# Optimization experiments

Measured on AMD Instinct MI355X. Metric: run time of the kernel, lower is better.

## Reference

```python
import jax, jax.numpy as jnp
import numpy as np

B = 32; NPG = 500; N = B * NPG; E = 256000; F = 1024; OD = 128
DD = 80; TD = 32; NH = 4; DH = TD // NH; DFF = 128; NL = 2
LSUB = 128; MAXLEN = 4 * LSUB
NEG = -1e9; SLOPE = 0.01; EPS = 1e-5


def setup_inputs() -> dict:
    key = jax.random.key(0)
    ks = iter(jax.random.split(key, 64))
    nrm = lambda *s: jax.random.normal(next(ks), s, jnp.float32)
    w = lambda *s: nrm(*s) * 0.02
    inp = {}
    inp["pro1_x"] = nrm(N, F)
    inp["pro2_x"] = nrm(N, F)
    inp["pro1_edge_index"] = jax.random.randint(next(ks), (2, E), 0, N)
    inp["pro2_edge_index"] = jax.random.randint(next(ks), (2, E), 0, N)
    inp["pro1_batch"] = jnp.repeat(jnp.arange(B), NPG)
    inp["pro2_batch"] = jnp.repeat(jnp.arange(B), NPG)
    for nm in ("mas1_straight", "mas1_flipped", "mas2_straight", "mas2_flipped"):
        inp[nm] = nrm(B, LSUB, DD)
        inp[nm + "_lengths"] = jax.random.randint(next(ks), (B,), 1, LSUB + 1)
    inp["gcn1_w"] = w(F, F); inp["gcn1_b"] = jnp.zeros(F)
    inp["gcn2_w"] = w(F, F); inp["gcn2_b"] = jnp.zeros(F)
    inp["fc1_w"] = w(OD, F); inp["fc1_b"] = jnp.zeros(OD)
    inp["fc2_w"] = w(OD, F); inp["fc2_b"] = jnp.zeros(OD)
    inp["red_w"] = w(TD - 2, DD); inp["red_b"] = jnp.zeros(TD - 2)
    inp["attn_in_w"] = w(NL, 3 * TD, TD); inp["attn_in_b"] = jnp.zeros((NL, 3 * TD))
    inp["attn_out_w"] = w(NL, TD, TD); inp["attn_out_b"] = jnp.zeros((NL, TD))
    inp["ln1_w"] = jnp.ones((NL, TD)); inp["ln1_b"] = jnp.zeros((NL, TD))
    inp["ln2_w"] = jnp.ones((NL, TD)); inp["ln2_b"] = jnp.zeros((NL, TD))
    inp["ff1_w"] = w(NL, DFF, TD); inp["ff1_b"] = jnp.zeros((NL, DFF))
    inp["ff2_w"] = w(NL, TD, DFF); inp["ff2_b"] = jnp.zeros((NL, TD))
    inp["final_w"] = w(1, 2 * OD + TD); inp["final_b"] = jnp.zeros(1)
    return inp


def _leaky(v):
    return jnp.where(v >= 0, v, SLOPE * v)


def _gcn(x, ei, W, b):
    # GCNConv: x' = D^-1/2 (A + I) D^-1/2 (x @ W^T) + b
    sl = jnp.arange(N, dtype=ei.dtype)
    src = jnp.concatenate([ei[0], sl])
    dst = jnp.concatenate([ei[1], sl])
    deg = jax.ops.segment_sum(jnp.ones(src.shape[0], x.dtype), dst, N)
    dinv = jax.lax.rsqrt(deg)
    norm = (dinv[src] * dinv[dst])[:, None]
    h = x @ W.T
    return jax.ops.segment_sum(h[src] * norm, dst, N) + b


def _gmp(x, batch):
    # global mean pool per graph
    s = jax.ops.segment_sum(x, batch, B)
    c = jax.ops.segment_sum(jnp.ones(x.shape[0], x.dtype), batch, B)
    return s / c[:, None]


def _ln(x, w, b):
    m = x.mean(-1, keepdims=True)
    v = ((x - m) ** 2).mean(-1, keepdims=True)
    return (x - m) * jax.lax.rsqrt(v + EPS) * w + b


def _forward(pro1_x, pro1_edge_index, pro1_batch, pro2_x, pro2_edge_index, pro2_batch,
             mas1_straight, mas1_flipped, mas2_straight, mas2_flipped,
             mas1_straight_lengths, mas1_flipped_lengths, mas2_straight_lengths, mas2_flipped_lengths,
             gcn1_w, gcn1_b, fc1_w, fc1_b, gcn2_w, gcn2_b, fc2_w, fc2_b,
             red_w, red_b, attn_in_w, attn_in_b, attn_out_w, attn_out_b,
             ln1_w, ln1_b, ln2_w, ln2_b, ff1_w, ff1_b, ff2_w, ff2_b,
             final_w, final_b):
    # --- graph branches (dropout = identity at inference) ---
    x1 = _leaky(_gcn(pro1_x, pro1_edge_index, gcn1_w, gcn1_b))
    x1 = _leaky(_gmp(x1, pro1_batch) @ fc1_w.T + fc1_b)           # [B, OD]
    x2 = _leaky(_gcn(pro2_x, pro2_edge_index, gcn2_w, gcn2_b))
    x2 = _leaky(_gmp(x2, pro2_batch) @ fc2_w.T + fc2_b)           # [B, OD]

    # --- vectorized ragged pack: project, append indicators, scatter to offsets ---
    inds = ((1.0, 1.0), (0.0, 1.0), (1.0, 0.0), (0.0, 0.0))      # (straight, first)
    mas = (mas1_straight, mas1_flipped, mas2_straight, mas2_flipped)
    lens = (mas1_straight_lengths, mas1_flipped_lengths, mas2_straight_lengths, mas2_flipped_lengths)
    pos = jnp.arange(LSUB)
    brow = jnp.arange(B)[:, None]
    seq = jnp.zeros((B, MAXLEN, TD), jnp.float32)
    off = jnp.zeros((B,), lens[0].dtype)
    for m, l, (si, fi) in zip(mas, lens, inds):
        proj = m @ red_w.T + red_b                                # [B, LSUB, TD-2]
        ones = jnp.ones((B, LSUB, 1), jnp.float32)
        p = jnp.concatenate([proj, si * ones, fi * ones], -1)    # [B, LSUB, TD]
        valid = pos[None, :] < l[:, None]                        # [B, LSUB]
        idx = jnp.where(valid, off[:, None] + pos[None, :], 0)
        seq = seq.at[brow, idx].add(p * valid[..., None])
        off = off + l
    mask = jnp.arange(MAXLEN)[None, :] < off[:, None]            # [B, MAXLEN] True = valid

    # --- post-norm TransformerEncoder (relu FFN, key padding mask) ---
    x_t = seq
    for li in range(NL):
        qkv = x_t @ attn_in_w[li].T + attn_in_b[li]
        q, k, v = jnp.split(qkv, 3, axis=-1)
        q = q.reshape(B, MAXLEN, NH, DH)
        k = k.reshape(B, MAXLEN, NH, DH)
        v = v.reshape(B, MAXLEN, NH, DH)
        scores = jnp.einsum('bqhd,bkhd->bhqk', q, k) / np.float32(np.sqrt(DH))
        scores = jnp.where(mask[:, None, None, :], scores, NEG)
        attn = jax.nn.softmax(scores, axis=-1)
        o = jnp.einsum('bhqk,bkhd->bqhd', attn, v).reshape(B, MAXLEN, TD)
        o = o @ attn_out_w[li].T + attn_out_b[li]
        x_t = _ln(x_t + o, ln1_w[li], ln1_b[li])
        h = jax.nn.relu(x_t @ ff1_w[li].T + ff1_b[li]) @ ff2_w[li].T + ff2_b[li]
        x_t = _ln(x_t + h, ln2_w[li], ln2_b[li])

    mf = mask[..., None].astype(jnp.float32)
    mas_out = (x_t * mf).sum(1) / mf.sum(1)                      # masked mean [B, TD]

    combined = jnp.concatenate([x1, x2, mas_out], axis=1)        # [B, 2*OD + TD]
    return combined @ final_w.T + final_b                        # [B, 1]


def reference(pro1_x, pro1_edge_index, pro1_batch, pro2_x, pro2_edge_index, pro2_batch,
              mas1_straight, mas1_flipped, mas2_straight, mas2_flipped,
              mas1_straight_lengths, mas1_flipped_lengths, mas2_straight_lengths, mas2_flipped_lengths,
              gcn1_w, gcn1_b, fc1_w, fc1_b, gcn2_w, gcn2_b, fc2_w, fc2_b,
              red_w, red_b, attn_in_w, attn_in_b, attn_out_w, attn_out_b,
              ln1_w, ln1_b, ln2_w, ln2_b, ff1_w, ff1_b, ff2_w, ff2_b,
              final_w, final_b):
    return _forward(pro1_x, pro1_edge_index, pro1_batch, pro2_x, pro2_edge_index, pro2_batch,
                    mas1_straight, mas1_flipped, mas2_straight, mas2_flipped,
                    mas1_straight_lengths, mas1_flipped_lengths, mas2_straight_lengths, mas2_flipped_lengths,
                    gcn1_w, gcn1_b, fc1_w, fc1_b, gcn2_w, gcn2_b, fc2_w, fc2_b,
                    red_w, red_b, attn_in_w, attn_in_b, attn_out_w, attn_out_b,
                    ln1_w, ln1_b, ln2_w, ln2_b, ff1_w, ff1_b, ff2_w, ff2_b,
                    final_w, final_b)
```

## Files before the change

kernel.cpp:

```cpp
#include <hip/hip_runtime.h>
#include <stdint.h>

#define N_NODES 16000
#define MPAD_   16128
#define B_      32
#define NPG_    500
#define E_      256000
#define F_      1024
#define OD_     128
#define DD_     80
#define TD_     32
#define NH_     4
#define DH_     8
#define DFF_    128
#define LSUB_   128
#define MAXLEN_ 512
#define EPS_    1e-5f
#define SLOPE_  0.01f

typedef __bf16 bf16x8 __attribute__((ext_vector_type(8)));
typedef float  f32x4  __attribute__((ext_vector_type(4)));

__device__ __forceinline__ float leaky(float v) { return v >= 0.f ? v : SLOPE_ * v; }

__device__ __forceinline__ unsigned short f2bf(float f) {
  unsigned u = __float_as_uint(f);
  u += 0x7FFFu + ((u >> 16) & 1u);
  return (unsigned short)(u >> 16);
}
__device__ __forceinline__ float bf2f(unsigned short u) {
  return __uint_as_float((unsigned)u << 16);
}
__device__ __forceinline__ float bflo(unsigned u) { return __uint_as_float(u << 16); }
__device__ __forceinline__ float bfhi(unsigned u) { return __uint_as_float(u & 0xffff0000u); }
__device__ __forceinline__ unsigned pk2bf(float lo, float hi) {
  return (unsigned)f2bf(lo) | ((unsigned)f2bf(hi) << 16);
}

__device__ __forceinline__ void gld_lds16(const void* g, void* l) {
  __builtin_amdgcn_global_load_lds(
      (const __attribute__((address_space(1))) unsigned int*)g,
      (__attribute__((address_space(3))) unsigned int*)l, 16, 0, 0);
}

__global__ void k_f2bf2(const float* __restrict__ in0, const float* __restrict__ in1,
                        unsigned short* __restrict__ out0, unsigned short* __restrict__ out1,
                        int n4) {
  const float* in = blockIdx.y ? in1 : in0;
  unsigned short* out = blockIdx.y ? out1 : out0;
  int i = blockIdx.x * blockDim.x + threadIdx.x;
  int stride = gridDim.x * blockDim.x;
  for (; i < n4; i += stride) {
    float4 v = ((const float4*)in)[i];
    ushort4 o;
    o.x = f2bf(v.x); o.y = f2bf(v.y); o.z = f2bf(v.z); o.w = f2bf(v.w);
    ((ushort4*)out)[i] = o;
  }
}

#define LDSA(bf, ks, row) (*(const bf16x8*)&lds[(bf)*16384 + (ks)*8192 + (row)*32 + rs])
#define LDSB(bf, ks, row) (*(const bf16x8*)&lds[32768 + (bf)*16384 + (ks)*8192 + (row)*32 + rs])
#define STG_A(bf, R, kti) do { \
  gld_lds16(&Ag[(size_t)(mBase + (R) + r4) * 1024 + (kti) * 64 + c4],      &lds[(bf)*16384 + (R)*32 + t*8]); \
  gld_lds16(&Ag[(size_t)(mBase + (R) + r4) * 1024 + (kti) * 64 + 32 + c4], &lds[(bf)*16384 + 8192 + (R)*32 + t*8]); \
} while (0)
#define STG_B(bf, R, kti) do { \
  gld_lds16(&Bg[(size_t)(nBase + (R) + r4) * 1024 + (kti) * 64 + c4],      &lds[32768 + (bf)*16384 + (R)*32 + t*8]); \
  gld_lds16(&Bg[(size_t)(nBase + (R) + r4) * 1024 + (kti) * 64 + 32 + c4], &lds[32768 + (bf)*16384 + 8192 + (R)*32 + t*8]); \
} while (0)
#define RD_Q0(bf) do { \
  _Pragma("unroll") for (int mi = 0; mi < 4; ++mi) \
  _Pragma("unroll") for (int ks = 0; ks < 2; ++ks) \
    aLo[mi][ks] = LDSA(bf, ks, wrow * 128 + mi * 16 + l15); \
  _Pragma("unroll") for (int ni = 0; ni < 2; ++ni) \
  _Pragma("unroll") for (int ks = 0; ks < 2; ++ks) \
    bLo[ni][ks] = LDSB(bf, ks, wcol * 64 + ni * 16 + l15); \
} while (0)
#define RD_BHI(bf) do { \
  _Pragma("unroll") for (int ni = 0; ni < 2; ++ni) \
  _Pragma("unroll") for (int ks = 0; ks < 2; ++ks) \
    bHi[ni][ks] = LDSB(bf, ks, wcol * 64 + (2 + ni) * 16 + l15); \
} while (0)
#define RD_AHI(bf) do { \
  _Pragma("unroll") for (int mi = 0; mi < 4; ++mi) \
  _Pragma("unroll") for (int ks = 0; ks < 2; ++ks) \
    aHi[mi][ks] = LDSA(bf, ks, wrow * 128 + (4 + mi) * 16 + l15); \
} while (0)
#define MM_Q0() do { __builtin_amdgcn_s_setprio(1); \
  _Pragma("unroll") for (int mi = 0; mi < 4; ++mi) \
  _Pragma("unroll") for (int ni = 0; ni < 2; ++ni) \
  _Pragma("unroll") for (int ks = 0; ks < 2; ++ks) \
    acc[mi][ni] = __builtin_amdgcn_mfma_f32_16x16x32_bf16(aLo[mi][ks], bLo[ni][ks], acc[mi][ni], 0, 0, 0); \
  __builtin_amdgcn_s_setprio(0); } while (0)
#define MM_Q1() do { __builtin_amdgcn_s_setprio(1); \
  _Pragma("unroll") for (int mi = 0; mi < 4; ++mi) \
  _Pragma("unroll") for (int ni = 0; ni < 2; ++ni) \
  _Pragma("unroll") for (int ks = 0; ks < 2; ++ks) \
    acc[mi][2 + ni] = __builtin_amdgcn_mfma_f32_16x16x32_bf16(aLo[mi][ks], bHi[ni][ks], acc[mi][2 + ni], 0, 0, 0); \
  __builtin_amdgcn_s_setprio(0); } while (0)
#define MM_Q3() do { __builtin_amdgcn_s_setprio(1); \
  _Pragma("unroll") for (int mi = 0; mi < 4; ++mi) \
  _Pragma("unroll") for (int ni = 0; ni < 2; ++ni) \
  _Pragma("unroll") for (int ks = 0; ks < 2; ++ks) \
    acc[4 + mi][2 + ni] = __builtin_amdgcn_mfma_f32_16x16x32_bf16(aHi[mi][ks], bHi[ni][ks], acc[4 + mi][2 + ni], 0, 0, 0); \
  __builtin_amdgcn_s_setprio(0); } while (0)
#define MM_Q2() do { __builtin_amdgcn_s_setprio(1); \
  _Pragma("unroll") for (int mi = 0; mi < 4; ++mi) \
  _Pragma("unroll") for (int ni = 0; ni < 2; ++ni) \
  _Pragma("unroll") for (int ks = 0; ks < 2; ++ks) \
    acc[4 + mi][ni] = __builtin_amdgcn_mfma_f32_16x16x32_bf16(aHi[mi][ks], bLo[ni][ks], acc[4 + mi][ni], 0, 0, 0); \
  __builtin_amdgcn_s_setprio(0); } while (0)
#define BAR() do { __builtin_amdgcn_sched_barrier(0); __builtin_amdgcn_s_barrier(); \
                   __builtin_amdgcn_sched_barrier(0); } while (0)
#define LGKM0() do { asm volatile("s_waitcnt lgkmcnt(0)" ::: "memory"); \
                     __builtin_amdgcn_sched_barrier(0); } while (0)
#define VM4() do { asm volatile("s_waitcnt vmcnt(4)" ::: "memory"); } while (0)
#define VM0() do { asm volatile("s_waitcnt vmcnt(0)" ::: "memory"); } while (0)

__global__ __launch_bounds__(512, 2) void k_gemm256(const unsigned short* __restrict__ Ag,
                                                    const unsigned short* __restrict__ Bg,
                                                    unsigned short* __restrict__ Cg) {
  __shared__ short lds[65536];
  const int j  = blockIdx.x;
  const int x8 = j & 7;
  const int chunk = (x8 < 4) ? x8 * 32 : 128 + (x8 - 4) * 31;
  const int pos = chunk + (j >> 3);
  const int mb = pos >> 2, nb = pos & 3;
  const size_t g = blockIdx.z;
  Ag += g * (size_t)MPAD_ * 1024;
  Bg += g * (size_t)1024 * 1024;
  Cg += g * (size_t)MPAD_ * 1024;
  const int t = threadIdx.x;
  const int lane = t & 63, wave = t >> 6;
  const int wrow = wave >> 2, wcol = wave & 3;
  const int quad = lane >> 4, l15 = lane & 15;
  const int mBase = mb * 256, nBase = nb * 256;
  const int r4 = t >> 2;
  const int c4 = (((t & 3) - ((t >> 3) & 3)) & 3) * 8;
  const int rs = ((quad + (l15 >> 1)) & 3) * 8;

  f32x4 acc[8][4];
  f32x4 zero = {0.f, 0.f, 0.f, 0.f};
#pragma unroll
  for (int i = 0; i < 8; ++i)
#pragma unroll
    for (int jn = 0; jn < 4; ++jn) acc[i][jn] = zero;

  bf16x8 aLo[4][2], aHi[4][2], bLo[2][2], bHi[2][2];

  STG_A(0, 0, 0); STG_A(0, 128, 0); STG_B(0, 0, 0); STG_B(0, 128, 0);
  STG_B(1, 0, 1); STG_B(1, 128, 1);
  VM4();
  BAR();

  for (int kt = 0; kt < 16; kt += 2) {
    const bool s2 = (kt + 2) < 16;
    const bool s3 = (kt + 3) < 16;
    RD_Q0(0);
    STG_A(1, 0, kt + 1);
    BAR(); LGKM0(); MM_Q0(); BAR();
    RD_BHI(0);
    STG_A(1, 128, kt + 1);
    BAR(); LGKM0(); MM_Q1(); BAR();
    RD_AHI(0);
    if (s2) STG_B(0, 0, kt + 2);
    BAR(); LGKM0(); MM_Q3(); BAR();
    if (s2) { STG_B(0, 128, kt + 2); VM4(); } else VM0();
    BAR(); MM_Q2(); BAR();
    RD_Q0(1);
    if (s2) STG_A(0, 0, kt + 2);
    BAR(); LGKM0(); MM_Q0(); BAR();
    RD_BHI(1);
    if (s2) STG_A(0, 128, kt + 2);
    BAR(); LGKM0(); MM_Q1(); BAR();
    RD_AHI(1);
    if (s3) STG_B(1, 0, kt + 3);
    BAR(); LGKM0(); MM_Q3(); BAR();
    if (s3) { STG_B(1, 128, kt + 3); VM4(); }
    BAR(); MM_Q2(); BAR();
  }

#pragma unroll
  for (int mi = 0; mi < 8; ++mi)
#pragma unroll
    for (int ni = 0; ni < 4; ++ni)
#pragma unroll
      for (int r = 0; r < 4; ++r) {
        int grow = mBase + wrow * 128 + mi * 16 + quad * 4 + r;
        int gcol = nBase + wcol * 64 + ni * 16 + l15;
        Cg[(size_t)grow * 1024 + gcol] = f2bf(acc[mi][ni][r]);
      }
}

__global__ void k_hist(const int* __restrict__ ei0, const int* __restrict__ ei1,
                       int* __restrict__ cnt, int e, int n) {
  const int g = blockIdx.y;
  const int* dst = (g ? ei1 : ei0) + e;
  int i = blockIdx.x * 256 + threadIdx.x;
  if (i < e) atomicAdd(&cnt[g * n + dst[i]], 1);
}

__global__ void k_scan(const int* __restrict__ cnt_all, int* __restrict__ rowstart_all,
                       int* __restrict__ cursor_all, float* __restrict__ dinv_all, int n) {
  const int g = blockIdx.x;
  const int* cnt = cnt_all + g * n;
  int* rowstart = rowstart_all + g * (n + 1);
  int* cursor   = cursor_all + g * n;
  float* dinv   = dinv_all + g * n;
  __shared__ int part[256];
  __shared__ int base[257];
  int t = threadIdx.x;
  int chunk = (n + 255) >> 8;
  int s = 0;
  for (int j = 0; j < chunk; ++j) {
    int idx = t * chunk + j;
    if (idx < n) s += cnt[idx];
  }
  part[t] = s;
  __syncthreads();
  if (t == 0) {
    int a = 0;
    for (int i = 0; i < 256; ++i) { base[i] = a; a += part[i]; }
    base[256] = a;
  }
  __syncthreads();
  int a = base[t];
  for (int j = 0; j < chunk; ++j) {
    int idx = t * chunk + j;
    if (idx < n) {
      int c = cnt[idx];
      rowstart[idx] = a; cursor[idx] = a; a += c;
      dinv[idx] = rsqrtf((float)c + 1.0f);
    }
  }
  if (t == 0) rowstart[n] = base[256];
}

__global__ void k_scatter(const int* __restrict__ ei0, const int* __restrict__ ei1,
                          const float* __restrict__ dinv_all, int* __restrict__ cursor_all,
                          int2* __restrict__ csre_all, int e, int n) {
  const int g = blockIdx.y;
  const int* ei = g ? ei1 : ei0;
  int i = blockIdx.x * 256 + threadIdx.x;
  if (i < e) {
    int s = ei[i], d = ei[e + i];
    int p = atomicAdd(&cursor_all[g * n + d], 1);
    float w = dinv_all[g * n + s] * dinv_all[g * n + d];
    csre_all[(size_t)g * e + p] = make_int2(s, __float_as_int(w));
  }
}

__global__ __launch_bounds__(256) void k_gather(const uint4* __restrict__ h8_all,
                                                const float* __restrict__ dinv_all,
                                                const int* __restrict__ rowstart_all,
                                                const int2* __restrict__ csre_all,
                                                uint4* __restrict__ agg8_all) {
  const int g = blockIdx.z;
  const uint4* h8 = h8_all + (size_t)g * MPAD_ * 128;
  const float* dinv = dinv_all + (size_t)g * N_NODES;
  const int* rowstart = rowstart_all + (size_t)g * (N_NODES + 1);
  const int2* csre = csre_all + (size_t)g * E_;
  uint4* agg8 = agg8_all + (size_t)g * N_NODES * 128;
  const int sl = blockIdx.x;
  const int t = threadIdx.x;
  const int wv = t >> 6, lane = t & 63;
  const int qtr = lane >> 4, l16 = lane & 15;
  const int i = blockIdx.y * 16 + wv * 4 + qtr;
  const int fo8 = sl * 16 + l16;
  const float di = dinv[i];
  const float selfw = di * di;
  uint4 sv = h8[(size_t)i * 128 + fo8];
  float a0 = bflo(sv.x) * selfw, a1 = bfhi(sv.x) * selfw;
  float a2 = bflo(sv.y) * selfw, a3 = bfhi(sv.y) * selfw;
  float a4 = bflo(sv.z) * selfw, a5 = bfhi(sv.z) * selfw;
  float a6 = bflo(sv.w) * selfw, a7 = bfhi(sv.w) * selfw;
  int j = rowstart[i];
  const int end = rowstart[i + 1];
  for (; j + 2 <= end; j += 2) {
    int2 e0 = csre[j], e1 = csre[j + 1];
    uint4 v0 = h8[(size_t)e0.x * 128 + fo8];
    uint4 v1 = h8[(size_t)e1.x * 128 + fo8];
    float w0 = __int_as_float(e0.y), w1 = __int_as_float(e1.y);
    a0 += bflo(v0.x) * w0 + bflo(v1.x) * w1;
    a1 += bfhi(v0.x) * w0 + bfhi(v1.x) * w1;
    a2 += bflo(v0.y) * w0 + bflo(v1.y) * w1;
    a3 += bfhi(v0.y) * w0 + bfhi(v1.y) * w1;
    a4 += bflo(v0.z) * w0 + bflo(v1.z) * w1;
    a5 += bfhi(v0.z) * w0 + bfhi(v1.z) * w1;
    a6 += bflo(v0.w) * w0 + bflo(v1.w) * w1;
    a7 += bfhi(v0.w) * w0 + bfhi(v1.w) * w1;
  }
  if (j < end) {
    int2 e0 = csre[j];
    uint4 v0 = h8[(size_t)e0.x * 128 + fo8];
    float w0 = __int_as_float(e0.y);
    a0 += bflo(v0.x) * w0; a1 += bfhi(v0.x) * w0;
    a2 += bflo(v0.y) * w0; a3 += bfhi(v0.y) * w0;
    a4 += bflo(v0.z) * w0; a5 += bfhi(v0.z) * w0;
    a6 += bflo(v0.w) * w0; a7 += bfhi(v0.w) * w0;
  }
  uint4 o;
  o.x = pk2bf(a0, a1); o.y = pk2bf(a2, a3);
  o.z = pk2bf(a4, a5); o.w = pk2bf(a6, a7);
  agg8[(size_t)i * 128 + fo8] = o;
}

__global__ void k_pool(const unsigned short* __restrict__ agg_all,
                       const float* __restrict__ bias0, const float* __restrict__ bias1,
                       float* __restrict__ pooled_all) {
  int f = blockIdx.x * 256 + threadIdx.x;
  int z = blockIdx.z;
  int g = z >> 5, b = z & 31;
  const unsigned short* agg = agg_all + (size_t)g * N_NODES * F_;
  const float* bias = g ? bias1 : bias0;
  float* pooled = pooled_all + (size_t)g * B_ * F_;
  int r0 = blockIdx.y * 100;
  float bf = bias[f];
  float s = 0.f;
  for (int r = 0; r < 100; ++r)
    s += leaky(bf2f(agg[(size_t)(b * NPG_ + r0 + r) * F_ + f]) + bf);
  atomicAdd(&pooled[b * F_ + f], s);
}

__global__ __launch_bounds__(256) void k_fc(const float* __restrict__ pooled_all,
                     const float* __restrict__ w0, const float* __restrict__ w1,
                     const float* __restrict__ bias0, const float* __restrict__ bias1,
                     float* __restrict__ out0, float* __restrict__ out1) {
  __shared__ float ps[F_];
  const int b = blockIdx.x, g = blockIdx.y, t = threadIdx.x;
  const float* p = pooled_all + (size_t)g * B_ * F_ + b * F_;
  const float* w = g ? w1 : w0;
  const float* bias = g ? bias1 : bias0;
  float* out = g ? out1 : out0;
  ((float4*)ps)[t] = ((const float4*)p)[t];
  __syncthreads();
  const int wave = t >> 6, lane = t & 63;
  for (int oo = 0; oo < 32; ++oo) {
    const int o = wave * 32 + oo;
    const float* wr = w + (size_t)o * F_;
    float a = 0.f;
#pragma unroll
    for (int c = 0; c < 16; ++c) a += wr[c * 64 + lane] * ps[c * 64 + lane];
#pragma unroll
    for (int m = 1; m < 64; m <<= 1) a += __shfl_xor(a, m, 64);
    if (lane == 0) out[b * OD_ + o] = leaky(a * (1.f / 500.f) + bias[o]);
  }
}

__global__ void k_pack(const float* __restrict__ m0, const float* __restrict__ m1,
                       const float* __restrict__ m2, const float* __restrict__ m3,
                       const int* __restrict__ l0, const int* __restrict__ l1,
                       const int* __restrict__ l2, const int* __restrict__ l3,
                       const float* __restrict__ rw, const float* __restrict__ rb,
                       float* __restrict__ seq) {
  __shared__ float xs[DD_];
  const int p = blockIdx.x, b = blockIdx.y, k = blockIdx.z;
  const float* mas = (k == 0) ? m0 : (k == 1) ? m1 : (k == 2) ? m2 : m3;
  const int*   lk  = (k == 0) ? l0 : (k == 1) ? l1 : (k == 2) ? l2 : l3;
  const int len = lk[b];
  if (p >= len) return;
  int off = 0;
  if (k > 0) off += l0[b];
  if (k > 1) off += l1[b];
  if (k > 2) off += l2[b];
  const int t = threadIdx.x;
  for (int d = t; d < DD_; d += 64) xs[d] = mas[(size_t)(b * LSUB_ + p) * DD_ + d];
  __syncthreads();
  if (t < TD_) {
    float v;
    if (t < TD_ - 2) {
      float a = rb[t];
      const float* w = &rw[t * DD_];
      for (int d = 0; d < DD_; ++d) a += xs[d] * w[d];
      v = a;
    } else if (t == TD_ - 2) {
      v = (k == 0 || k == 2) ? 1.f : 0.f;
    } else {
      v = (k < 2) ? 1.f : 0.f;
    }
    seq[((size_t)b * MAXLEN_ + off + p) * TD_ + t] = v;
  }
}

__global__ void k_totlen(const int* __restrict__ l0, const int* __restrict__ l1,
                         const int* __restrict__ l2, const int* __restrict__ l3,
                         int* __restrict__ tot) {
  int b = threadIdx.x;
  if (b < B_) tot[b] = l0[b] + l1[b] + l2[b] + l3[b];
}

__global__ void k_qkv(const float* __restrict__ xt, const float* __restrict__ w,
                      const float* __restrict__ bias, const int* __restrict__ tot,
                      float* __restrict__ qkv) {
  __shared__ float xs[TD_];
  const int row = blockIdx.x;
  if ((row & (MAXLEN_ - 1)) >= tot[row >> 9]) return;
  const int t = threadIdx.x;
  if (t < TD_) xs[t] = xt[(size_t)row * TD_ + t];
  __syncthreads();
  if (t < 3 * TD_) {
    float a = bias[t];
    const float* wr = &w[t * TD_];
#pragma unroll
    for (int k = 0; k < TD_; ++k) a += xs[k] * wr[k];
    qkv[(size_t)row * 96 + t] = a;
  }
}

__global__ __launch_bounds__(128) void k_attn(const float* __restrict__ qkv,
                                              const int* __restrict__ tot,
                                              float* __restrict__ obuf) {
  __shared__ float Kl[MAXLEN_ * DH_];
  __shared__ float Vl[MAXLEN_ * DH_];
  const int h = blockIdx.x, b = blockIdx.y, qz = blockIdx.z;
  const int t = threadIdx.x;
  const int L = tot[b];
  if (qz * 64 >= L) return;
  const float* base = &qkv[(size_t)b * MAXLEN_ * 96];
  for (int i = t; i < L * DH_; i += 128) {
    int p = i >> 3, d = i & 7;
    Kl[i] = base[p * 96 + 32 + h * 8 + d];
    Vl[i] = base[p * 96 + 64 + h * 8 + d];
  }
  __syncthreads();
  const int qi = qz * 64 + (t >> 1);
  if (qi >= L) return;
  const int half = t & 1;
  const float scale = 0.35355339059327373f;
  float q[8];
#pragma unroll
  for (int d = 0; d < 8; ++d) q[d] = base[qi * 96 + h * 8 + d] * scale;

  float l0 = 0.f, l1 = 0.f;
  float a0[8] = {0, 0, 0, 0, 0, 0, 0, 0};
  float a1[8] = {0, 0, 0, 0, 0, 0, 0, 0};
  int j = half;
  for (; j + 2 < L; j += 4) {
    const float* kr0 = &Kl[j * 8];
    const float* kr1 = &Kl[(j + 2) * 8];
    float s0 = 0.f, s1 = 0.f;
#pragma unroll
    for (int d = 0; d < 8; ++d) { s0 += q[d] * kr0[d]; s1 += q[d] * kr1[d]; }
    float p0 = __expf(s0), p1 = __expf(s1);
    l0 += p0; l1 += p1;
    const float* vr0 = &Vl[j * 8];
    const float* vr1 = &Vl[(j + 2) * 8];
#pragma unroll
    for (int d = 0; d < 8; ++d) { a0[d] += p0 * vr0[d]; a1[d] += p1 * vr1[d]; }
  }
  for (; j < L; j += 2) {
    const float* kr = &Kl[j * 8];
    float s = 0.f;
#pragma unroll
    for (int d = 0; d < 8; ++d) s += q[d] * kr[d];
    float p = __expf(s);
    l0 += p;
    const float* vr = &Vl[j * 8];
#pragma unroll
    for (int d = 0; d < 8; ++d) a0[d] += p * vr[d];
  }
  float l = l0 + l1;
#pragma unroll
  for (int d = 0; d < 8; ++d) a0[d] += a1[d];
  l += __shfl_xor(l, 1);
#pragma unroll
  for (int d = 0; d < 8; ++d) a0[d] += __shfl_xor(a0[d], 1);
  float inv = 1.f / l;
  const int dbase = half * 4;
  float4 o;
  o.x = a0[dbase + 0] * inv; o.y = a0[dbase + 1] * inv;
  o.z = a0[dbase + 2] * inv; o.w = a0[dbase + 3] * inv;
  *(float4*)&obuf[((size_t)b * MAXLEN_ + qi) * TD_ + h * 8 + dbase] = o;
}

__global__ __launch_bounds__(128) void k_post(const float* __restrict__ obuf,
                                              const float* __restrict__ ow,
                                              const float* __restrict__ ob,
                                              const float* __restrict__ l1w,
                                              const float* __restrict__ l1b,
                                              const float* __restrict__ f1w,
                                              const float* __restrict__ f1b,
                                              const float* __restrict__ f2w,
                                              const float* __restrict__ f2b,
                                              const float* __restrict__ l2w,
                                              const float* __restrict__ l2b,
                                              const int* __restrict__ tot,
                                              float* __restrict__ xt) {
  const int r = blockIdx.x, t = threadIdx.x;
  if ((r & (MAXLEN_ - 1)) >= tot[r >> 9]) return;
  __shared__ float xs[TD_];
  __shared__ float hb[DFF_];
  if (t < TD_) {
    const float* orow = &obuf[(size_t)r * TD_];
    float a = ob[t] + xt[(size_t)r * TD_ + t];
    const float* wr = &ow[t * TD_];
#pragma unroll
    for (int k = 0; k < TD_; ++k) a += orow[k] * wr[k];
    float s1 = a, s2 = a * a;
#pragma unroll
    for (int m = 1; m < 32; m <<= 1) {
      s1 += __shfl_xor(s1, m, 32);
      s2 += __shfl_xor(s2, m, 32);
    }
    float mean = s1 * (1.f / 32.f);
    float var  = s2 * (1.f / 32.f) - mean * mean;
    xs[t] = (a - mean) * rsqrtf(var + EPS_) * l1w[t] + l1b[t];
  }
  __syncthreads();
  {
    float a = f1b[t];
    const float* wr = &f1w[t * TD_];
#pragma unroll
    for (int k = 0; k < TD_; ++k) a += xs[k] * wr[k];
    hb[t] = fmaxf(a, 0.f);
  }
  __syncthreads();
  if (t < TD_) {
    float a = f2b[t] + xs[t];
    const float* wr = &f2w[t * DFF_];
#pragma unroll
    for (int k = 0; k < DFF_; ++k) a += hb[k] * wr[k];
    float s1 = a, s2 = a * a;
#pragma unroll
    for (int m = 1; m < 32; m <<= 1) {
      s1 += __shfl_xor(s1, m, 32);
      s2 += __shfl_xor(s2, m, 32);
    }
    float mean = s1 * (1.f / 32.f);
    float var  = s2 * (1.f / 32.f) - mean * mean;
    xt[(size_t)r * TD_ + t] = (a - mean) * rsqrtf(var + EPS_) * l2w[t] + l2b[t];
  }
}

__global__ __launch_bounds__(256) void k_maskfinal(const float* __restrict__ xt,
                                                   const int* __restrict__ tot,
                                                   const float* __restrict__ x1,
                                                   const float* __restrict__ x2,
                                                   const float* __restrict__ fw,
                                                   const float* __restrict__ fb,
                                                   float* __restrict__ out) {
  __shared__ float sbuf[8][32];
  __shared__ float mo[TD_];
  const int b = blockIdx.x, t = threadIdx.x;
  const int j = t & 31, c = t >> 5;
  const int L = tot[b];
  float s = 0.f;
  for (int p = c; p < L; p += 8) s += xt[((size_t)b * MAXLEN_ + p) * TD_ + j];
  sbuf[c][j] = s;
  __syncthreads();
  if (t < 32) {
    float a = 0.f;
#pragma unroll
    for (int cc = 0; cc < 8; ++cc) a += sbuf[cc][t];
    mo[t] = a / (float)L;
  }
  __syncthreads();
  if (t < 64) {
    float s2 = 0.f;
    for (int i = t; i < 2 * OD_ + TD_; i += 64) {
      float cv = (i < OD_) ? x1[b * OD_ + i]
               : (i < 2 * OD_) ? x2[b * OD_ + (i - OD_)]
               : mo[i - 2 * OD_];
      s2 += fw[i] * cv;
    }
#pragma unroll
    for (int m = 1; m < 64; m <<= 1) s2 += __shfl_xor(s2, m, 64);
    if (t == 0) out[b] = s2 + fb[0];
  }
}

extern "C" void kernel_launch(void* const* d_in, const int* in_sizes, int n_in,
                              void* d_out, int out_size, void* d_ws, size_t ws_size,
                              hipStream_t stream) {
  (void)in_sizes; (void)n_in; (void)out_size; (void)ws_size;
  const float* pro_x[2]  = {(const float*)d_in[0], (const float*)d_in[1]};
  const int*   pro_ei[2] = {(const int*)d_in[2], (const int*)d_in[3]};
  const float* mas[4]    = {(const float*)d_in[6], (const float*)d_in[8],
                            (const float*)d_in[10], (const float*)d_in[12]};
  const int*   lens[4]   = {(const int*)d_in[7], (const int*)d_in[9],
                            (const int*)d_in[11], (const int*)d_in[13]};
  const float* gw[2]  = {(const float*)d_in[14], (const float*)d_in[16]};
  const float* gb[2]  = {(const float*)d_in[15], (const float*)d_in[17]};
  const float* fcw[2] = {(const float*)d_in[18], (const float*)d_in[20]};
  const float* fcb[2] = {(const float*)d_in[19], (const float*)d_in[21]};
  const float* red_w = (const float*)d_in[22];
  const float* red_b = (const float*)d_in[23];
  const float* attn_in_w  = (const float*)d_in[24];
  const float* attn_in_b  = (const float*)d_in[25];
  const float* attn_out_w = (const float*)d_in[26];
  const float* attn_out_b = (const float*)d_in[27];
  const float* ln1_w = (const float*)d_in[28];
  const float* ln1_b = (const float*)d_in[29];
  const float* ln2_w = (const float*)d_in[30];
  const float* ln2_b = (const float*)d_in[31];
  const float* ff1_w = (const float*)d_in[32];
  const float* ff1_b = (const float*)d_in[33];
  const float* ff2_w = (const float*)d_in[34];
  const float* ff2_b = (const float*)d_in[35];
  const float* final_w = (const float*)d_in[36];
  const float* final_b = (const float*)d_in[37];
  float* out = (float*)d_out;

  char* p = (char*)d_ws;
  auto carve = [&](size_t bytes) -> void* {
    void* r = (void*)p;
    p += (bytes + 255) & ~(size_t)255;
    return r;
  };
  unsigned short* xb  = (unsigned short*)carve((size_t)2 * MPAD_ * F_ * 2);
  unsigned short* Wb  = (unsigned short*)carve((size_t)2 * F_ * F_ * 2);
  unsigned short* h   = (unsigned short*)carve((size_t)2 * MPAD_ * F_ * 2);
  unsigned short* agg = (unsigned short*)carve((size_t)2 * N_NODES * F_ * 2);
  int*   cnt      = (int*)carve((size_t)2 * N_NODES * 4);
  float* dinv     = (float*)carve((size_t)2 * N_NODES * 4);
  int*   rowstart = (int*)carve((size_t)2 * (N_NODES + 1) * 4);
  int*   cursor   = (int*)carve((size_t)2 * N_NODES * 4);
  int2*  csre     = (int2*)carve((size_t)2 * E_ * 8);
  float* pooled   = (float*)carve((size_t)2 * B_ * F_ * 4);
  float* xg[2];
  xg[0] = (float*)carve((size_t)B_ * OD_ * 4);
  xg[1] = (float*)carve((size_t)B_ * OD_ * 4);
  float* seq    = (float*)carve((size_t)B_ * MAXLEN_ * TD_ * 4);
  float* qkv    = (float*)carve((size_t)B_ * MAXLEN_ * 96 * 4);
  float* obuf   = (float*)carve((size_t)B_ * MAXLEN_ * TD_ * 4);
  int*   totlen = (int*)carve((size_t)B_ * 4);

  k_f2bf2<<<dim3(1024, 2), 256, 0, stream>>>(pro_x[0], pro_x[1], xb,
                                             xb + (size_t)MPAD_ * F_, (N_NODES * F_) / 4);
  k_f2bf2<<<dim3(512, 2), 256, 0, stream>>>(gw[0], gw[1], Wb, Wb + (size_t)F_ * F_,
                                            (F_ * F_) / 4);
  k_gemm256<<<dim3(252, 1, 2), 512, 0, stream>>>(xb, Wb, h);
  hipMemsetAsync(cnt, 0, (size_t)2 * N_NODES * 4, stream);
  k_hist<<<dim3(1000, 2), 256, 0, stream>>>(pro_ei[0], pro_ei[1], cnt, E_, N_NODES);
  k_scan<<<2, 256, 0, stream>>>(cnt, rowstart, cursor, dinv, N_NODES);
  k_scatter<<<dim3(1000, 2), 256, 0, stream>>>(pro_ei[0], pro_ei[1], dinv, cursor,
                                               csre, E_, N_NODES);
  k_gather<<<dim3(8, 1000, 2), 256, 0, stream>>>((const uint4*)h, dinv, rowstart,
                                                 csre, (uint4*)agg);
  hipMemsetAsync(pooled, 0, (size_t)2 * B_ * F_ * 4, stream);
  k_pool<<<dim3(4, 5, 64), 256, 0, stream>>>(agg, gb[0], gb[1], pooled);
  k_fc<<<dim3(B_, 2), 256, 0, stream>>>(pooled, fcw[0], fcw[1], fcb[0], fcb[1],
                                        xg[0], xg[1]);

  k_pack<<<dim3(LSUB_, B_, 4), 64, 0, stream>>>(mas[0], mas[1], mas[2], mas[3],
                                                lens[0], lens[1], lens[2], lens[3],
                                                red_w, red_b, seq);
  k_totlen<<<1, 64, 0, stream>>>(lens[0], lens[1], lens[2], lens[3], totlen);

  for (int li = 0; li < 2; ++li) {
    k_qkv<<<B_ * MAXLEN_, 128, 0, stream>>>(seq, attn_in_w + (size_t)li * 96 * TD_,
                                            attn_in_b + (size_t)li * 96, totlen, qkv);
    k_attn<<<dim3(NH_, B_, 8), 128, 0, stream>>>(qkv, totlen, obuf);
    k_post<<<B_ * MAXLEN_, 128, 0, stream>>>(
        obuf, attn_out_w + (size_t)li * TD_ * TD_, attn_out_b + (size_t)li * TD_,
        ln1_w + (size_t)li * TD_, ln1_b + (size_t)li * TD_,
        ff1_w + (size_t)li * DFF_ * TD_, ff1_b + (size_t)li * DFF_,
        ff2_w + (size_t)li * TD_ * DFF_, ff2_b + (size_t)li * TD_,
        ln2_w + (size_t)li * TD_, ln2_b + (size_t)li * TD_, totlen, seq);
  }

  k_maskfinal<<<B_, 256, 0, stream>>>(seq, totlen, xg[0], xg[1], final_w, final_b, out);
}
```

Baseline: 734.0 us.

## Merge prep kernels, slice-major agg layout, atomic-free pooling, split QKV layout

Merges the two bf16 conversion launches and the count memset into one kernel, and folds the total-length computation into the pack kernel. The gather now writes aggregates with nontemporal stores in a feature-slice-major layout. A new pooling kernel writes per-chunk partial sums that the FC kernel reduces, replacing the atomics and the pooled memset. QKV is split into separate Q, K and V buffers with a head-major K/V layout so attention can load K/V with float4 copies, and QKV launches process four rows per block. Together these cut launch count and uncoalesced access, at the cost of more buffers and some code complexity.

```diff
diff --git a/kernel.cpp b/kernel.cpp
--- a/kernel.cpp
+++ b/kernel.cpp
@@ -20,6 +20,7 @@
 
 typedef __bf16 bf16x8 __attribute__((ext_vector_type(8)));
 typedef float  f32x4  __attribute__((ext_vector_type(4)));
+typedef unsigned u32x4 __attribute__((ext_vector_type(4)));
 
 __device__ __forceinline__ float leaky(float v) { return v >= 0.f ? v : SLOPE_ * v; }
 
@@ -43,13 +44,22 @@
       (__attribute__((address_space(3))) unsigned int*)l, 16, 0, 0);
 }
 
-__global__ void k_f2bf2(const float* __restrict__ in0, const float* __restrict__ in1,
-                        unsigned short* __restrict__ out0, unsigned short* __restrict__ out1,
-                        int n4) {
-  const float* in = blockIdx.y ? in1 : in0;
-  unsigned short* out = blockIdx.y ? out1 : out0;
-  int i = blockIdx.x * blockDim.x + threadIdx.x;
-  int stride = gridDim.x * blockDim.x;
+__global__ void k_prep(const float* __restrict__ x0, const float* __restrict__ x1,
+                       const float* __restrict__ w0, const float* __restrict__ w1,
+                       unsigned short* __restrict__ xb0, unsigned short* __restrict__ xb1,
+                       unsigned short* __restrict__ wb0, unsigned short* __restrict__ wb1,
+                       int* __restrict__ cnt) {
+  const int y = blockIdx.y;
+  int i = blockIdx.x * 256 + threadIdx.x;
+  const int stride = gridDim.x * 256;
+  if (y == 4) {
+    int4 z = make_int4(0, 0, 0, 0);
+    for (; i < (2 * N_NODES) / 4; i += stride) ((int4*)cnt)[i] = z;
+    return;
+  }
+  const float* in = (y == 0) ? x0 : (y == 1) ? x1 : (y == 2) ? w0 : w1;
+  unsigned short* out = (y == 0) ? xb0 : (y == 1) ? xb1 : (y == 2) ? wb0 : wb1;
+  const int n4 = (y < 2) ? (N_NODES * F_ / 4) : (F_ * F_ / 4);
   for (; i < n4; i += stride) {
     float4 v = ((const float4*)in)[i];
     ushort4 o;
@@ -254,13 +264,12 @@
                                                 const float* __restrict__ dinv_all,
                                                 const int* __restrict__ rowstart_all,
                                                 const int2* __restrict__ csre_all,
-                                                uint4* __restrict__ agg8_all) {
+                                                unsigned* __restrict__ aggs_all) {
   const int g = blockIdx.z;
   const uint4* h8 = h8_all + (size_t)g * MPAD_ * 128;
   const float* dinv = dinv_all + (size_t)g * N_NODES;
   const int* rowstart = rowstart_all + (size_t)g * (N_NODES + 1);
   const int2* csre = csre_all + (size_t)g * E_;
-  uint4* agg8 = agg8_all + (size_t)g * N_NODES * 128;
   const int sl = blockIdx.x;
   const int t = threadIdx.x;
   const int wv = t >> 6, lane = t & 63;
@@ -299,40 +308,49 @@
     a4 += bflo(v0.z) * w0; a5 += bfhi(v0.z) * w0;
     a6 += bflo(v0.w) * w0; a7 += bfhi(v0.w) * w0;
   }
-  uint4 o;
+  u32x4 o;
   o.x = pk2bf(a0, a1); o.y = pk2bf(a2, a3);
   o.z = pk2bf(a4, a5); o.w = pk2bf(a6, a7);
-  agg8[(size_t)i * 128 + fo8] = o;
-}
-
-__global__ void k_pool(const unsigned short* __restrict__ agg_all,
-                       const float* __restrict__ bias0, const float* __restrict__ bias1,
-                       float* __restrict__ pooled_all) {
-  int f = blockIdx.x * 256 + threadIdx.x;
-  int z = blockIdx.z;
-  int g = z >> 5, b = z & 31;
-  const unsigned short* agg = agg_all + (size_t)g * N_NODES * F_;
+  u32x4* dst = (u32x4*)&aggs_all[(((size_t)(g * 8 + sl) * N_NODES + i) * 16 + l16) * 4];
+  __builtin_nontemporal_store(o, dst);
+}
+
+__global__ __launch_bounds__(512) void k_poolpart(const unsigned short* __restrict__ aggs,
+                                                  const float* __restrict__ bias0,
+                                                  const float* __restrict__ bias1,
+                                                  float* __restrict__ partial) {
+  const int b = blockIdx.x, g = blockIdx.y, c = blockIdx.z;
+  const int t = threadIdx.x;
+  const int sl = t >> 6, o = t & 63;
   const float* bias = g ? bias1 : bias0;
-  float* pooled = pooled_all + (size_t)g * B_ * F_;
-  int r0 = blockIdx.y * 100;
-  float bf = bias[f];
-  float s = 0.f;
-  for (int r = 0; r < 100; ++r)
-    s += leaky(bf2f(agg[(size_t)(b * NPG_ + r0 + r) * F_ + f]) + bf);
-  atomicAdd(&pooled[b * F_ + f], s);
-}
-
-__global__ __launch_bounds__(256) void k_fc(const float* __restrict__ pooled_all,
+  const float bf0 = bias[t * 2], bf1 = bias[t * 2 + 1];
+  const ushort2* base = (const ushort2*)aggs + ((size_t)(g * 8 + sl) * N_NODES) * 64 + o;
+  const int r0 = b * NPG_ + c * 100;
+  float s0 = 0.f, s1 = 0.f;
+  for (int r = 0; r < 100; ++r) {
+    ushort2 v = base[(size_t)(r0 + r) * 64];
+    s0 += leaky(bf2f(v.x) + bf0);
+    s1 += leaky(bf2f(v.y) + bf1);
+  }
+  *(float2*)&partial[(((size_t)c * 2 + g) * B_ + b) * F_ + t * 2] = make_float2(s0, s1);
+}
+
+__global__ __launch_bounds__(256) void k_fc(const float* __restrict__ partial,
                      const float* __restrict__ w0, const float* __restrict__ w1,
                      const float* __restrict__ bias0, const float* __restrict__ bias1,
                      float* __restrict__ out0, float* __restrict__ out1) {
   __shared__ float ps[F_];
   const int b = blockIdx.x, g = blockIdx.y, t = threadIdx.x;
-  const float* p = pooled_all + (size_t)g * B_ * F_ + b * F_;
   const float* w = g ? w1 : w0;
   const float* bias = g ? bias1 : bias0;
   float* out = g ? out1 : out0;
-  ((float4*)ps)[t] = ((const float4*)p)[t];
+  float4 s = {0.f, 0.f, 0.f, 0.f};
+#pragma unroll
+  for (int c = 0; c < 5; ++c) {
+    float4 v = ((const float4*)(partial + (((size_t)c * 2 + g) * B_ + b) * F_))[t];
+    s.x += v.x; s.y += v.y; s.z += v.z; s.w += v.w;
+  }
+  ((float4*)ps)[t] = s;
   __syncthreads();
   const int wave = t >> 6, lane = t & 63;
   for (int oo = 0; oo < 32; ++oo) {
@@ -352,7 +370,7 @@
                        const int* __restrict__ l0, const int* __restrict__ l1,
                        const int* __restrict__ l2, const int* __restrict__ l3,
                        const float* __restrict__ rw, const float* __restrict__ rb,
-                       float* __restrict__ seq) {
+                       float* __restrict__ seq, int* __restrict__ tot) {
   __shared__ float xs[DD_];
   const int p = blockIdx.x, b = blockIdx.y, k = blockIdx.z;
   const float* mas = (k == 0) ? m0 : (k == 1) ? m1 : (k == 2) ? m2 : m3;
@@ -364,6 +382,7 @@
   if (k > 1) off += l1[b];
   if (k > 2) off += l2[b];
   const int t = threadIdx.x;
+  if (p == 0 && k == 0 && t == 63) tot[b] = l0[b] + l1[b] + l2[b] + l3[b];
   for (int d = t; d < DD_; d += 64) xs[d] = mas[(size_t)(b * LSUB_ + p) * DD_ + d];
   __syncthreads();
   if (t < TD_) {
@@ -382,32 +401,40 @@
   }
 }
 
-__global__ void k_totlen(const int* __restrict__ l0, const int* __restrict__ l1,
-                         const int* __restrict__ l2, const int* __restrict__ l3,
-                         int* __restrict__ tot) {
-  int b = threadIdx.x;
-  if (b < B_) tot[b] = l0[b] + l1[b] + l2[b] + l3[b];
-}
-
-__global__ void k_qkv(const float* __restrict__ xt, const float* __restrict__ w,
-                      const float* __restrict__ bias, const int* __restrict__ tot,
-                      float* __restrict__ qkv) {
-  __shared__ float xs[TD_];
-  const int row = blockIdx.x;
-  if ((row & (MAXLEN_ - 1)) >= tot[row >> 9]) return;
-  const int t = threadIdx.x;
-  if (t < TD_) xs[t] = xt[(size_t)row * TD_ + t];
-  __syncthreads();
-  if (t < 3 * TD_) {
-    float a = bias[t];
-    const float* wr = &w[t * TD_];
-#pragma unroll
-    for (int k = 0; k < TD_; ++k) a += xs[k] * wr[k];
-    qkv[(size_t)row * 96 + t] = a;
-  }
-}
-
-__global__ __launch_bounds__(128) void k_attn(const float* __restrict__ qkv,
+__global__ __launch_bounds__(512) void k_qkv(const float* __restrict__ xt,
+                                             const float* __restrict__ w,
+                                             const float* __restrict__ bias,
+                                             const int* __restrict__ tot,
+                                             float* __restrict__ Qp,
+                                             float* __restrict__ Kp,
+                                             float* __restrict__ Vp) {
+  __shared__ float xs[4][TD_];
+  const int u = threadIdx.x >> 7;
+  const int t = threadIdx.x & 127;
+  const int row = blockIdx.x * 4 + u;
+  const int b = row >> 9, p = row & (MAXLEN_ - 1);
+  const bool alive = p < tot[b];
+  if (alive && t < TD_) xs[u][t] = xt[(size_t)row * TD_ + t];
+  __syncthreads();
+  if (!alive || t >= 3 * TD_) return;
+  float a = bias[t];
+  const float* wr = &w[t * TD_];
+#pragma unroll
+  for (int k = 0; k < TD_; ++k) a += xs[u][k] * wr[k];
+  if (t < 32) {
+    Qp[(size_t)row * 32 + t] = a;
+  } else if (t < 64) {
+    int h = (t - 32) >> 3, d = (t - 32) & 7;
+    Kp[(((size_t)b * NH_ + h) * MAXLEN_ + p) * DH_ + d] = a;
+  } else {
+    int h = (t - 64) >> 3, d = (t - 64) & 7;
+    Vp[(((size_t)b * NH_ + h) * MAXLEN_ + p) * DH_ + d] = a;
+  }
+}
+
+__global__ __launch_bounds__(128) void k_attn(const float* __restrict__ Qp,
+                                              const float* __restrict__ Kp,
+                                              const float* __restrict__ Vp,
                                               const int* __restrict__ tot,
                                               float* __restrict__ obuf) {
   __shared__ float Kl[MAXLEN_ * DH_];
@@ -416,11 +443,12 @@
   const int t = threadIdx.x;
   const int L = tot[b];
   if (qz * 64 >= L) return;
-  const float* base = &qkv[(size_t)b * MAXLEN_ * 96];
-  for (int i = t; i < L * DH_; i += 128) {
-    int p = i >> 3, d = i & 7;
-    Kl[i] = base[p * 96 + 32 + h * 8 + d];
-    Vl[i] = base[p * 96 + 64 + h * 8 + d];
+  const float* Kpl = Kp + ((size_t)b * NH_ + h) * MAXLEN_ * DH_;
+  const float* Vpl = Vp + ((size_t)b * NH_ + h) * MAXLEN_ * DH_;
+  const int n4 = (L * DH_ + 3) >> 2;
+  for (int i = t; i < n4; i += 128) {
+    ((float4*)Kl)[i] = ((const float4*)Kpl)[i];
+    ((float4*)Vl)[i] = ((const float4*)Vpl)[i];
   }
   __syncthreads();
   const int qi = qz * 64 + (t >> 1);
@@ -429,7 +457,7 @@
   const float scale = 0.35355339059327373f;
   float q[8];
 #pragma unroll
-  for (int d = 0; d < 8; ++d) q[d] = base[qi * 96 + h * 8 + d] * scale;
+  for (int d = 0; d < 8; ++d) q[d] = Qp[((size_t)b * MAXLEN_ + qi) * TD_ + h * 8 + d] * scale;
 
   float l0 = 0.f, l1 = 0.f;
   float a0[8] = {0, 0, 0, 0, 0, 0, 0, 0};
@@ -610,47 +638,46 @@
   unsigned short* xb  = (unsigned short*)carve((size_t)2 * MPAD_ * F_ * 2);
   unsigned short* Wb  = (unsigned short*)carve((size_t)2 * F_ * F_ * 2);
   unsigned short* h   = (unsigned short*)carve((size_t)2 * MPAD_ * F_ * 2);
-  unsigned short* agg = (unsigned short*)carve((size_t)2 * N_NODES * F_ * 2);
+  unsigned short* aggs = (unsigned short*)carve((size_t)2 * 8 * N_NODES * 128 * 2);
   int*   cnt      = (int*)carve((size_t)2 * N_NODES * 4);
   float* dinv     = (float*)carve((size_t)2 * N_NODES * 4);
   int*   rowstart = (int*)carve((size_t)2 * (N_NODES + 1) * 4);
   int*   cursor   = (int*)carve((size_t)2 * N_NODES * 4);
   int2*  csre     = (int2*)carve((size_t)2 * E_ * 8);
-  float* pooled   = (float*)carve((size_t)2 * B_ * F_ * 4);
+  float* partial  = (float*)carve((size_t)5 * 2 * B_ * F_ * 4);
   float* xg[2];
   xg[0] = (float*)carve((size_t)B_ * OD_ * 4);
   xg[1] = (float*)carve((size_t)B_ * OD_ * 4);
   float* seq    = (float*)carve((size_t)B_ * MAXLEN_ * TD_ * 4);
-  float* qkv    = (float*)carve((size_t)B_ * MAXLEN_ * 96 * 4);
+  float* Qp     = (float*)carve((size_t)B_ * MAXLEN_ * TD_ * 4);
+  float* Kp     = (float*)carve((size_t)B_ * NH_ * MAXLEN_ * DH_ * 4);
+  float* Vp     = (float*)carve((size_t)B_ * NH_ * MAXLEN_ * DH_ * 4);
   float* obuf   = (float*)carve((size_t)B_ * MAXLEN_ * TD_ * 4);
   int*   totlen = (int*)carve((size_t)B_ * 4);
 
-  k_f2bf2<<<dim3(1024, 2), 256, 0, stream>>>(pro_x[0], pro_x[1], xb,
-                                             xb + (size_t)MPAD_ * F_, (N_NODES * F_) / 4);
-  k_f2bf2<<<dim3(512, 2), 256, 0, stream>>>(gw[0], gw[1], Wb, Wb + (size_t)F_ * F_,
-                                            (F_ * F_) / 4);
+  k_prep<<<dim3(1024, 5), 256, 0, stream>>>(pro_x[0], pro_x[1], gw[0], gw[1],
+                                            xb, xb + (size_t)MPAD_ * F_,
+                                            Wb, Wb + (size_t)F_ * F_, cnt);
   k_gemm256<<<dim3(252, 1, 2), 512, 0, stream>>>(xb, Wb, h);
-  hipMemsetAsync(cnt, 0, (size_t)2 * N_NODES * 4, stream);
   k_hist<<<dim3(1000, 2), 256, 0, stream>>>(pro_ei[0], pro_ei[1], cnt, E_, N_NODES);
   k_scan<<<2, 256, 0, stream>>>(cnt, rowstart, cursor, dinv, N_NODES);
   k_scatter<<<dim3(1000, 2), 256, 0, stream>>>(pro_ei[0], pro_ei[1], dinv, cursor,
                                                csre, E_, N_NODES);
   k_gather<<<dim3(8, 1000, 2), 256, 0, stream>>>((const uint4*)h, dinv, rowstart,
-                                                 csre, (uint4*)agg);
-  hipMemsetAsync(pooled, 0, (size_t)2 * B_ * F_ * 4, stream);
-  k_pool<<<dim3(4, 5, 64), 256, 0, stream>>>(agg, gb[0], gb[1], pooled);
-  k_fc<<<dim3(B_, 2), 256, 0, stream>>>(pooled, fcw[0], fcw[1], fcb[0], fcb[1],
+                                                 csre, (unsigned*)aggs);
+  k_poolpart<<<dim3(B_, 2, 5), 512, 0, stream>>>(aggs, gb[0], gb[1], partial);
+  k_fc<<<dim3(B_, 2), 256, 0, stream>>>(partial, fcw[0], fcw[1], fcb[0], fcb[1],
                                         xg[0], xg[1]);
 
   k_pack<<<dim3(LSUB_, B_, 4), 64, 0, stream>>>(mas[0], mas[1], mas[2], mas[3],
                                                 lens[0], lens[1], lens[2], lens[3],
-                                                red_w, red_b, seq);
-  k_totlen<<<1, 64, 0, stream>>>(lens[0], lens[1], lens[2], lens[3], totlen);
+                                                red_w, red_b, seq, totlen);
 
   for (int li = 0; li < 2; ++li) {
-    k_qkv<<<B_ * MAXLEN_, 128, 0, stream>>>(seq, attn_in_w + (size_t)li * 96 * TD_,
-                                            attn_in_b + (size_t)li * 96, totlen, qkv);
-    k_attn<<<dim3(NH_, B_, 8), 128, 0, stream>>>(qkv, totlen, obuf);
+    k_qkv<<<(B_ * MAXLEN_) / 4, 512, 0, stream>>>(seq, attn_in_w + (size_t)li * 96 * TD_,
+                                                  attn_in_b + (size_t)li * 96, totlen,
+                                                  Qp, Kp, Vp);
+    k_attn<<<dim3(NH_, B_, 8), 128, 0, stream>>>(Qp, Kp, Vp, totlen, obuf);
     k_post<<<B_ * MAXLEN_, 128, 0, stream>>>(
         obuf, attn_out_w + (size_t)li * TD_ * TD_, attn_out_b + (size_t)li * TD_,
         ln1_w + (size_t)li * TD_, ln1_b + (size_t)li * TD_,
```

Measured after the change: 721.2 us. Within noise of the previous version (-1.7%).
